# Kernel optimization log

Hardware: AMD Instinct MI355X
Metric: run time of the kernel (lower is better)

Reference implementation:

```python
import jax, jax.numpy as jnp
import numpy as np

B, L, D, H, DH = 2, 2048, 768, 12, 3072
HD = D // H          # head dim = 64
EPS = 1e-6
SCALE = float(np.sqrt(HD))


def setup_inputs() -> dict:
    key = jax.random.key(0)
    ks = jax.random.split(key, 24)
    w = lambda k, shape: jax.random.normal(k, shape, jnp.float32) * 0.02
    # RoPE angles: [L, HD//2]
    inv_freq = 1.0 / (10000.0 ** (jnp.arange(HD // 2, dtype=jnp.float32) / (HD // 2)))
    ang = jnp.arange(L, dtype=jnp.float32)[:, None] * inv_freq[None, :]
    return {
        "x": jax.random.normal(ks[0], (B, L, D), jnp.float32),
        "c": jax.random.normal(ks[1], (B, D), jnp.float32),
        "freqs_cos": jnp.cos(ang),
        "freqs_sin": jnp.sin(ang),
        "W_q": w(ks[2], (D, D)), "W_k": w(ks[3], (D, D)),
        "W_v": w(ks[4], (D, D)), "W_o": w(ks[5], (D, D)),
        "cond_w1": w(ks[6], (D, DH)), "cond_b1": jnp.zeros((DH,), jnp.float32),
        "cond_w2": w(ks[7], (DH, D)), "cond_b2": jnp.zeros((D,), jnp.float32),
        "attn_norm_w": jnp.ones((D,), jnp.float32),
        "attn_alpha": w(ks[8], (D, D)), "attn_beta": w(ks[9], (D, D)),
        "attn_gamma": w(ks[10], (D, D)),
        "ffn_gate": w(ks[11], (D, DH)), "ffn_hidden": w(ks[12], (D, DH)),
        "ffn_out": w(ks[13], (DH, D)),
        "ffn_norm_w": jnp.ones((D,), jnp.float32),
        "ffn_beta": w(ks[14], (D, D)), "ffn_gamma": w(ks[15], (D, D)),
    }


def _rms_norm(x, w):
    return w * x * jax.lax.rsqrt(jnp.mean(x * x, axis=-1, keepdims=True) + EPS)


def _rope(x, cos, sin):
    # x: [b, n, l, hd]; complex pairs are consecutive (even, odd) lanes
    x0, x1 = x[..., 0::2], x[..., 1::2]
    c, s = cos[None, None], sin[None, None]          # [1,1,l,hd//2]
    r0 = x0 * c - x1 * s
    r1 = x0 * s + x1 * c
    return jnp.stack([r0, r1], axis=-1).reshape(x.shape)


def _attention(h, cos, sin, W_q, W_k, W_v, W_o):
    b, l, d = h.shape
    split = lambda y: y.reshape(b, l, H, HD).transpose(0, 2, 1, 3)  # b n l hd
    q = _rope(split(h @ W_q), cos, sin)
    k = _rope(split(h @ W_k), cos, sin)
    v = split(h @ W_v)
    scores = jnp.einsum("bnld,bnmd->bnlm", q, k) / SCALE
    attn = jax.nn.softmax(scores, axis=-1)
    o = jnp.einsum("bnlm,bnmd->bnld", attn, v)
    return o.transpose(0, 2, 1, 3).reshape(b, l, d) @ W_o


def reference(x, c, freqs_cos, freqs_sin, W_q, W_k, W_v, W_o,
              cond_w1, cond_b1, cond_w2, cond_b2,
              attn_norm_w, attn_alpha, attn_beta, attn_gamma,
              ffn_gate, ffn_hidden, ffn_out, ffn_norm_w, ffn_beta, ffn_gamma):
    # conditioning embedding
    c2 = jax.nn.silu(c @ cond_w1 + cond_b1) @ cond_w2 + cond_b2   # [b, d]
    mod = lambda W: (c2 @ W)[:, None]                              # [b, 1, d]
    # attention sub-block with AdaLN modulation + alpha gating
    h = _rms_norm(x, attn_norm_w) * mod(attn_gamma) + mod(attn_beta)
    x = x + _attention(h, freqs_cos, freqs_sin, W_q, W_k, W_v, W_o) * mod(attn_alpha)
    # SwiGLU FFN sub-block (original gates the residual by ffn_gamma, not alpha)
    h = _rms_norm(x, ffn_norm_w) * mod(ffn_gamma) + mod(ffn_beta)
    ff = (jax.nn.silu(h @ ffn_gate) * (h @ ffn_hidden)) @ ffn_out
    return x + ff * mod(ffn_gamma)
```

## Files before the change

kernel.cpp:

```cpp
#include <hip/hip_runtime.h>

typedef unsigned short u16;
typedef __attribute__((ext_vector_type(8))) short short8;
typedef __attribute__((ext_vector_type(4))) float f32x4;

#define L_SEQ 2048
#define NHEAD 12

__device__ __forceinline__ u16 f2bf(float f) {
    union { float f; unsigned u; } x; x.f = f;
    unsigned r = x.u + 0x7fffu + ((x.u >> 16) & 1u);
    return (u16)(r >> 16);
}
__device__ __forceinline__ float bf2f(u16 u) {
    union { unsigned u; float f; } x; x.u = ((unsigned)u) << 16;
    return x.f;
}
__device__ __forceinline__ float silu_f(float x) { return x / (1.f + __expf(-x)); }

__device__ __forceinline__ void gload16(const u16* g, u16* l) {
    __builtin_amdgcn_global_load_lds(
        (const __attribute__((address_space(1))) void*)g,
        (__attribute__((address_space(3))) void*)l, 16, 0, 0);
}

__global__ __launch_bounds__(256) void transpose_convert4(
    const float* __restrict__ S0, const float* __restrict__ S1,
    const float* __restrict__ S2, const float* __restrict__ S3,
    u16* __restrict__ D0, u16* __restrict__ D1, u16* __restrict__ D2, u16* __restrict__ D3,
    int K, int N)
{
    const float* W = (blockIdx.z == 0) ? S0 : (blockIdx.z == 1) ? S1 : (blockIdx.z == 2) ? S2 : S3;
    u16* Wt = (blockIdx.z == 0) ? D0 : (blockIdx.z == 1) ? D1 : (blockIdx.z == 2) ? D2 : D3;
    __shared__ float t[32][33];
    int tx = threadIdx.x & 31, ty = threadIdx.x >> 5;
    int n0 = blockIdx.x * 32, k0 = blockIdx.y * 32;
#pragma unroll
    for (int i = 0; i < 4; i++)
        t[ty + 8 * i][tx] = W[(size_t)(k0 + ty + 8 * i) * N + n0 + tx];
    __syncthreads();
#pragma unroll
    for (int i = 0; i < 4; i++)
        Wt[(size_t)(n0 + ty + 8 * i) * K + k0 + tx] = f2bf(t[tx][ty + 8 * i]);
}

__global__ __launch_bounds__(256) void cond_mlp1(
    const float* __restrict__ c, const float* __restrict__ w1, float* __restrict__ part)
{
    int j = blockIdx.x * 256 + threadIdx.x;
    int d0 = blockIdx.y * 96;
    float a0 = 0.f, a1 = 0.f;
    for (int d = d0; d < d0 + 96; ++d) {
        float w = w1[(size_t)d * 3072 + j];
        a0 += c[d] * w;
        a1 += c[768 + d] * w;
    }
    part[(size_t)(blockIdx.y * 2 + 0) * 3072 + j] = a0;
    part[(size_t)(blockIdx.y * 2 + 1) * 3072 + j] = a1;
}

__global__ __launch_bounds__(256) void cond_mlp2(
    const float* __restrict__ part, const float* __restrict__ b1,
    const float* __restrict__ w2, float* __restrict__ c2part)
{
    __shared__ float hid[2][384];
    const int tid = threadIdx.x;
    const int d0 = blockIdx.y * 384;
    for (int i = tid; i < 768; i += 256) {
        int b = i / 384, dd = i - b * 384;
        float s = b1[d0 + dd];
#pragma unroll
        for (int p = 0; p < 8; p++) s += part[(size_t)(p * 2 + b) * 3072 + d0 + dd];
        hid[b][dd] = silu_f(s);
    }
    __syncthreads();
    int jj = tid & 63, kc = tid >> 6;
    int j = blockIdx.x * 64 + jj;
    float a0 = 0.f, a1 = 0.f;
    for (int dd = kc * 96; dd < kc * 96 + 96; ++dd) {
        float w = w2[(size_t)(d0 + dd) * 768 + j];
        a0 += hid[0][dd] * w;
        a1 += hid[1][dd] * w;
    }
    __shared__ float r0[256], r1[256];
    r0[tid] = a0; r1[tid] = a1;
    __syncthreads();
    if (kc == 0) {
        a0 = r0[jj] + r0[64 + jj] + r0[128 + jj] + r0[192 + jj];
        a1 = r1[jj] + r1[64 + jj] + r1[128 + jj] + r1[192 + jj];
        c2part[(size_t)(blockIdx.y * 2 + 0) * 768 + j] = a0;
        c2part[(size_t)(blockIdx.y * 2 + 1) * 768 + j] = a1;
    }
}

__global__ __launch_bounds__(256) void mod_gemm(
    const float* __restrict__ c2part, const float* __restrict__ b2,
    const float* __restrict__ W0, const float* __restrict__ W1,
    const float* __restrict__ W2, const float* __restrict__ W3,
    const float* __restrict__ W4, float* __restrict__ out)
{
    __shared__ float c2s[2][768];
    const int tid = threadIdx.x;
    for (int i = tid; i < 1536; i += 256) {
        int b = i / 768, d = i - b * 768;
        float s = b2[d];
#pragma unroll
        for (int p = 0; p < 8; p++) s += c2part[(size_t)(p * 2 + b) * 768 + d];
        c2s[b][d] = s;
    }
    __syncthreads();
    int w = blockIdx.y;
    const float* W = (w == 0) ? W0 : (w == 1) ? W1 : (w == 2) ? W2 : (w == 3) ? W3 : W4;
    int jj = tid & 63, kc = tid >> 6;
    int j = blockIdx.x * 64 + jj;
    float a0 = 0.f, a1 = 0.f;
    for (int d = kc * 192; d < kc * 192 + 192; ++d) {
        float ww = W[(size_t)d * 768 + j];
        a0 += c2s[0][d] * ww;
        a1 += c2s[1][d] * ww;
    }
    __shared__ float r0[256], r1[256];
    r0[tid] = a0; r1[tid] = a1;
    __syncthreads();
    if (kc == 0) {
        a0 = r0[jj] + r0[64 + jj] + r0[128 + jj] + r0[192 + jj];
        a1 = r1[jj] + r1[64 + jj] + r1[128 + jj] + r1[192 + jj];
        out[(size_t)(w * 2 + 0) * 768 + j] = a0;
        out[(size_t)(w * 2 + 1) * 768 + j] = a1;
    }
}

__global__ __launch_bounds__(256) void rmsnorm_mod(
    const float* __restrict__ xin, const float* __restrict__ nw,
    const float* __restrict__ gamma, const float* __restrict__ beta,
    u16* __restrict__ hout)
{
    int row = blockIdx.x;
    int b = row >> 11;
    const float* xr = xin + (size_t)row * 768;
    int t = threadIdx.x;
    float v0 = xr[t], v1 = xr[t + 256], v2 = xr[t + 512];
    float ss = v0 * v0 + v1 * v1 + v2 * v2;
#pragma unroll
    for (int m = 1; m < 64; m <<= 1) ss += __shfl_xor(ss, m);
    __shared__ float red[4];
    if ((t & 63) == 0) red[t >> 6] = ss;
    __syncthreads();
    float tot = red[0] + red[1] + red[2] + red[3];
    float rr = rsqrtf(tot * (1.f / 768.f) + 1e-6f);
    u16* ho = hout + (size_t)row * 768;
    const float* g = gamma + (size_t)b * 768;
    const float* be = beta + (size_t)b * 768;
#pragma unroll
    for (int i = 0; i < 3; i++) {
        int col = t + i * 256;
        float v = (i == 0) ? v0 : (i == 1) ? v1 : v2;
        ho[col] = f2bf(v * rr * nw[col] * g[col] + be[col]);
    }
}

template<int BM, int WM, int MODE>
__global__ __launch_bounds__(256) void gemm_bf16(
    const u16* __restrict__ A,
    const u16* __restrict__ B0, const u16* __restrict__ B1, const u16* __restrict__ B2,
    float* __restrict__ Cf, u16* __restrict__ Cb,
    const float* __restrict__ X, const float* __restrict__ coef,
    int M, int N, int K)
{
    constexpr int MR = WM / 16, NR = 4;
    __shared__ __align__(16) u16 As[2][BM * 32];
    __shared__ __align__(16) u16 Bs[2][128 * 32];
    const u16* Bt = (blockIdx.z == 0) ? B0 : ((blockIdx.z == 1) ? B1 : B2);
    const size_t zoff = (size_t)blockIdx.z * (size_t)M * (size_t)N;
    const int tid = threadIdx.x;
    const int lane = tid & 63, wid = tid >> 6;
    const int lo = lane & 15, hi = lane >> 4;
    const int bm = blockIdx.x * BM, bn = blockIdx.y * 128;
    const int wrow = (wid >> 1) * WM, wcol = (wid & 1) * 64;

    f32x4 acc[MR][NR];
#pragma unroll
    for (int a = 0; a < MR; a++)
#pragma unroll
        for (int b = 0; b < NR; b++)
            acc[a][b] = (f32x4){0.f, 0.f, 0.f, 0.f};

    auto stage = [&](int buf, int k0) {
#pragma unroll
        for (int p = 0; p < BM / 64; p++) {
            int ch = tid + p * 256;
            gload16(A + (size_t)(bm + (ch >> 2)) * K + k0 + (ch & 3) * 8, &As[buf][ch * 8]);
        }
#pragma unroll
        for (int p = 0; p < 2; p++) {
            int ch = tid + p * 256;
            gload16(Bt + (size_t)(bn + (ch >> 2)) * K + k0 + (ch & 3) * 8, &Bs[buf][ch * 8]);
        }
    };

    stage(0, 0);
    int cur = 0;
    const int NT = K >> 5;
    for (int t = 0; t < NT; t++) {
        __syncthreads();
        if (t + 1 < NT) stage(cur ^ 1, (t + 1) * 32);
        short8 af[MR], bfr[NR];
#pragma unroll
        for (int mi = 0; mi < MR; mi++)
            af[mi] = *(const short8*)(&As[cur][(wrow + mi * 16 + lo) * 32 + hi * 8]);
#pragma unroll
        for (int nj = 0; nj < NR; nj++)
            bfr[nj] = *(const short8*)(&Bs[cur][(wcol + nj * 16 + lo) * 32 + hi * 8]);
        __builtin_amdgcn_s_setprio(1);
#pragma unroll
        for (int mi = 0; mi < MR; mi++)
#pragma unroll
            for (int nj = 0; nj < NR; nj++)
                acc[mi][nj] = __builtin_amdgcn_mfma_f32_16x16x32_bf16(af[mi], bfr[nj], acc[mi][nj], 0, 0, 0);
        __builtin_amdgcn_s_setprio(0);
        cur ^= 1;
    }
#pragma unroll
    for (int mi = 0; mi < MR; mi++)
#pragma unroll
        for (int nj = 0; nj < NR; nj++)
#pragma unroll
            for (int i = 0; i < 4; i++) {
                int row = bm + wrow + mi * 16 + hi * 4 + i;
                int col = bn + wcol + nj * 16 + lo;
                size_t idx = (size_t)row * N + col;
                float v = acc[mi][nj][i];
                if (MODE == 1) {
                    Cb[zoff + idx] = f2bf(v);
                } else {
                    int b = row >> 11;
                    Cf[idx] = X[idx] + v * coef[(size_t)b * N + col];
                }
            }
}

__global__ __launch_bounds__(256) void gemm_ffn1(
    const u16* __restrict__ A, const u16* __restrict__ Gt, const u16* __restrict__ Ht,
    u16* __restrict__ ff, int M, int N, int K)
{
    __shared__ __align__(16) u16 As[2][128 * 32];
    __shared__ __align__(16) u16 Gs[2][64 * 32];
    __shared__ __align__(16) u16 Hs[2][64 * 32];
    const int tid = threadIdx.x;
    const int lane = tid & 63, wid = tid >> 6;
    const int lo = lane & 15, hi = lane >> 4;
    const int bm = blockIdx.x * 128, bn = blockIdx.y * 64;
    const int wrow = (wid >> 1) * 64, wcol = (wid & 1) * 32;

    f32x4 ag[4][2], ah[4][2];
#pragma unroll
    for (int a = 0; a < 4; a++)
#pragma unroll
        for (int b = 0; b < 2; b++) {
            ag[a][b] = (f32x4){0.f, 0.f, 0.f, 0.f};
            ah[a][b] = (f32x4){0.f, 0.f, 0.f, 0.f};
        }

    auto stage = [&](int buf, int k0) {
#pragma unroll
        for (int p = 0; p < 2; p++) {
            int ch = tid + p * 256;
            gload16(A + (size_t)(bm + (ch >> 2)) * K + k0 + (ch & 3) * 8, &As[buf][ch * 8]);
        }
        {
            int ch = tid;
            gload16(Gt + (size_t)(bn + (ch >> 2)) * K + k0 + (ch & 3) * 8, &Gs[buf][ch * 8]);
            gload16(Ht + (size_t)(bn + (ch >> 2)) * K + k0 + (ch & 3) * 8, &Hs[buf][ch * 8]);
        }
    };

    stage(0, 0);
    int cur = 0;
    const int NT = K >> 5;
    for (int t = 0; t < NT; t++) {
        __syncthreads();
        if (t + 1 < NT) stage(cur ^ 1, (t + 1) * 32);
        short8 af[4], gf[2], hf[2];
#pragma unroll
        for (int mi = 0; mi < 4; mi++)
            af[mi] = *(const short8*)(&As[cur][(wrow + mi * 16 + lo) * 32 + hi * 8]);
#pragma unroll
        for (int nj = 0; nj < 2; nj++) {
            gf[nj] = *(const short8*)(&Gs[cur][(wcol + nj * 16 + lo) * 32 + hi * 8]);
            hf[nj] = *(const short8*)(&Hs[cur][(wcol + nj * 16 + lo) * 32 + hi * 8]);
        }
        __builtin_amdgcn_s_setprio(1);
#pragma unroll
        for (int mi = 0; mi < 4; mi++)
#pragma unroll
            for (int nj = 0; nj < 2; nj++) {
                ag[mi][nj] = __builtin_amdgcn_mfma_f32_16x16x32_bf16(af[mi], gf[nj], ag[mi][nj], 0, 0, 0);
                ah[mi][nj] = __builtin_amdgcn_mfma_f32_16x16x32_bf16(af[mi], hf[nj], ah[mi][nj], 0, 0, 0);
            }
        __builtin_amdgcn_s_setprio(0);
        cur ^= 1;
    }
#pragma unroll
    for (int mi = 0; mi < 4; mi++)
#pragma unroll
        for (int nj = 0; nj < 2; nj++)
#pragma unroll
            for (int i = 0; i < 4; i++) {
                int row = bm + wrow + mi * 16 + hi * 4 + i;
                int col = bn + wcol + nj * 16 + lo;
                ff[(size_t)row * N + col] = f2bf(silu_f(ag[mi][nj][i]) * ah[mi][nj][i]);
            }
}

__global__ __launch_bounds__(256) void rope_reshape(
    const u16* __restrict__ qr, const u16* __restrict__ kr, const u16* __restrict__ vr,
    const float* __restrict__ fc, const float* __restrict__ fs,
    u16* __restrict__ qo, u16* __restrict__ ko, u16* __restrict__ vt)
{
    const float QSCALE = 0.125f * 1.44269504f;
    __shared__ u16 Vl[64 * 64];
    const int tid = threadIdx.x;
    const int bh = blockIdx.y, lt = blockIdx.x;
    const int b = bh / NHEAD, h = bh % NHEAD;
    const int l0 = lt * 64;
    const int lrow = tid >> 2, ch = tid & 3;

    const size_t srow = ((size_t)(b * L_SEQ + l0 + lrow)) * 768 + h * 64 + ch * 16;
    const size_t drow = ((size_t)(bh * L_SEQ + l0 + lrow)) * 64 + ch * 16;

    float cs[8], sn[8];
#pragma unroll
    for (int i = 0; i < 8; i++) {
        cs[i] = fc[(l0 + lrow) * 32 + ch * 8 + i];
        sn[i] = fs[(l0 + lrow) * 32 + ch * 8 + i];
    }
    union { int4 v4[2]; u16 s[16]; } iv, ov;
    iv.v4[0] = *(const int4*)(qr + srow); iv.v4[1] = *(const int4*)(qr + srow + 8);
#pragma unroll
    for (int i = 0; i < 8; i++) {
        float x0 = bf2f(iv.s[2 * i]), x1 = bf2f(iv.s[2 * i + 1]);
        ov.s[2 * i]     = f2bf((x0 * cs[i] - x1 * sn[i]) * QSCALE);
        ov.s[2 * i + 1] = f2bf((x0 * sn[i] + x1 * cs[i]) * QSCALE);
    }
    *(int4*)(qo + drow) = ov.v4[0]; *(int4*)(qo + drow + 8) = ov.v4[1];
    iv.v4[0] = *(const int4*)(kr + srow); iv.v4[1] = *(const int4*)(kr + srow + 8);
#pragma unroll
    for (int i = 0; i < 8; i++) {
        float x0 = bf2f(iv.s[2 * i]), x1 = bf2f(iv.s[2 * i + 1]);
        ov.s[2 * i]     = f2bf(x0 * cs[i] - x1 * sn[i]);
        ov.s[2 * i + 1] = f2bf(x0 * sn[i] + x1 * cs[i]);
    }
    *(int4*)(ko + drow) = ov.v4[0]; *(int4*)(ko + drow + 8) = ov.v4[1];
    iv.v4[0] = *(const int4*)(vr + srow); iv.v4[1] = *(const int4*)(vr + srow + 8);
#pragma unroll
    for (int e = 0; e < 16; e++) {
        int d = ch * 16 + e;
        Vl[d * 64 + (lrow ^ (((d >> 3) & 7) << 3))] = iv.s[e];
    }
    __syncthreads();
    const int d = tid >> 2;
    const int key = ((d >> 3) & 7) << 3;
    int4 o0 = *(const int4*)(&Vl[d * 64 + ((ch * 16) ^ key)]);
    int4 o1 = *(const int4*)(&Vl[d * 64 + ((ch * 16 + 8) ^ key)]);
    u16* vd = vt + ((size_t)bh * 64 + d) * L_SEQ + l0 + ch * 16;
    *(int4*)(vd) = o0; *(int4*)(vd + 8) = o1;
}

__global__ __launch_bounds__(256) void attn_fwd(
    const u16* __restrict__ q, const u16* __restrict__ k, const u16* __restrict__ vt,
    u16* __restrict__ outp)
{
    __shared__ __align__(16) u16 Kb[2][64 * 64];
    __shared__ __align__(16) u16 Vb[2][64 * 64];
    __shared__ __align__(16) u16 Ps[4][16 * 64];
    const int tid = threadIdx.x;
    const int lane = tid & 63, wid = tid >> 6;
    const int lo = lane & 15, hi = lane >> 4;
    const int qt = blockIdx.x, bh = blockIdx.y;
    const int b = bh / NHEAD, h = bh % NHEAD;
    const int q0 = qt * 64 + wid * 16;
    const u16* qb = q + ((size_t)bh * L_SEQ + q0) * 64;
    const u16* kbase = k + (size_t)bh * L_SEQ * 64;
    const u16* vbase = vt + (size_t)bh * 64 * L_SEQ;

    short8 qa0 = *(const short8*)(qb + lo * 64 + hi * 8);
    short8 qa1 = *(const short8*)(qb + lo * 64 + 32 + hi * 8);

    f32x4 oacc[4];
#pragma unroll
    for (int dt = 0; dt < 4; dt++) oacc[dt] = (f32x4){0.f, 0.f, 0.f, 0.f};
    float m_ = -1e30f, ls = 0.f;

    auto stage = [&](int buf, int kv0) {
#pragma unroll
        for (int p = 0; p < 2; p++) {
            int chk = tid + p * 256;
            int r = chk >> 3;
            int sl = (chk & 7) ^ (r & 7);
            gload16(kbase + (size_t)(kv0 + r) * 64 + sl * 8, &Kb[buf][chk * 8]);
        }
#pragma unroll
        for (int p = 0; p < 2; p++) {
            int chk = tid + p * 256;
            int r = chk >> 3;
            int sl = (chk & 7) ^ (r & 7);
            gload16(vbase + (size_t)r * L_SEQ + kv0 + sl * 8, &Vb[buf][chk * 8]);
        }
    };

    stage(0, 0);
    int cur = 0;
    u16* pw = &Ps[wid][0];
    const int pkey = (lo & 7) << 3;
    for (int t = 0; t < L_SEQ / 64; t++) {
        __syncthreads();
        if (t + 1 < L_SEQ / 64) stage(cur ^ 1, (t + 1) * 64);
        f32x4 s[4];
#pragma unroll
        for (int nt = 0; nt < 4; nt++) {
            int kr = nt * 16 + lo;
            const u16* kp = &Kb[cur][kr * 64];
            short8 kf0 = *(const short8*)(kp + ((hi * 8) ^ pkey));
            short8 kf1 = *(const short8*)(kp + ((32 + hi * 8) ^ pkey));
            __builtin_amdgcn_s_setprio(1);
            f32x4 z = (f32x4){0.f, 0.f, 0.f, 0.f};
            z = __builtin_amdgcn_mfma_f32_16x16x32_bf16(kf0, qa0, z, 0, 0, 0);
            s[nt] = __builtin_amdgcn_mfma_f32_16x16x32_bf16(kf1, qa1, s[nt] = z, 0, 0, 0);
            __builtin_amdgcn_s_setprio(0);
        }
        float t0 = fmaxf(fmaxf(s[0][0], s[0][1]), fmaxf(s[0][2], s[0][3]));
        float t1 = fmaxf(fmaxf(s[1][0], s[1][1]), fmaxf(s[1][2], s[1][3]));
        float t2 = fmaxf(fmaxf(s[2][0], s[2][1]), fmaxf(s[2][2], s[2][3]));
        float t3 = fmaxf(fmaxf(s[3][0], s[3][1]), fmaxf(s[3][2], s[3][3]));
        float pmax = fmaxf(fmaxf(t0, t1), fmaxf(t2, t3));
        pmax = fmaxf(pmax, __shfl_xor(pmax, 16));
        pmax = fmaxf(pmax, __shfl_xor(pmax, 32));
        if (!__all(pmax - m_ <= 8.f)) {
            float mn = fmaxf(m_, pmax);
            float al = exp2f(m_ - mn);
            m_ = mn;
            ls *= al;
#pragma unroll
            for (int dt = 0; dt < 4; dt++) oacc[dt] *= al;
        }
        float rs = 0.f;
#pragma unroll
        for (int nt = 0; nt < 4; nt++)
#pragma unroll
            for (int r = 0; r < 4; r++) {
                float p = exp2f(s[nt][r] - m_);
                s[nt][r] = p;
                rs += p;
            }
        rs += __shfl_xor(rs, 16);
        rs += __shfl_xor(rs, 32);
        ls += rs;
#pragma unroll
        for (int nt = 0; nt < 4; nt++) {
            unsigned w0, w1;
            asm("v_cvt_pk_bf16_f32 %0, %1, %2" : "=v"(w0) : "v"(s[nt][0]), "v"(s[nt][1]));
            asm("v_cvt_pk_bf16_f32 %0, %1, %2" : "=v"(w1) : "v"(s[nt][2]), "v"(s[nt][3]));
            uint2 pk2; pk2.x = w0; pk2.y = w1;
            *(uint2*)(pw + lo * 64 + ((nt * 16 + hi * 4) ^ pkey)) = pk2;
        }
        short8 pa0 = *(const short8*)(pw + lo * 64 + ((hi * 8) ^ pkey));
        short8 pa1 = *(const short8*)(pw + lo * 64 + ((32 + hi * 8) ^ pkey));
#pragma unroll
        for (int dt = 0; dt < 4; dt++) {
            int vr_ = dt * 16 + lo;
            const u16* vp = &Vb[cur][vr_ * 64];
            short8 vf0 = *(const short8*)(vp + ((hi * 8) ^ pkey));
            short8 vf1 = *(const short8*)(vp + ((32 + hi * 8) ^ pkey));
            __builtin_amdgcn_s_setprio(1);
            oacc[dt] = __builtin_amdgcn_mfma_f32_16x16x32_bf16(vf0, pa0, oacc[dt], 0, 0, 0);
            oacc[dt] = __builtin_amdgcn_mfma_f32_16x16x32_bf16(vf1, pa1, oacc[dt], 0, 0, 0);
            __builtin_amdgcn_s_setprio(0);
        }
        cur ^= 1;
    }
    float inv = 1.f / ls;
    int qrow = q0 + lo;
    u16* orow = outp + ((size_t)(b * L_SEQ + qrow)) * 768 + h * 64;
#pragma unroll
    for (int dt = 0; dt < 4; dt++)
#pragma unroll
        for (int r = 0; r < 4; r++)
            orow[dt * 16 + hi * 4 + r] = f2bf(oacc[dt][r] * inv);
}

extern "C" void kernel_launch(void* const* d_in, const int* in_sizes, int n_in,
                              void* d_out, int out_size, void* d_ws, size_t ws_size,
                              hipStream_t stream)
{
    const float* x      = (const float*)d_in[0];
    const float* c      = (const float*)d_in[1];
    const float* fcos   = (const float*)d_in[2];
    const float* fsin   = (const float*)d_in[3];
    const float* Wq     = (const float*)d_in[4];
    const float* Wk     = (const float*)d_in[5];
    const float* Wv     = (const float*)d_in[6];
    const float* Wo     = (const float*)d_in[7];
    const float* cw1    = (const float*)d_in[8];
    const float* cb1    = (const float*)d_in[9];
    const float* cw2    = (const float*)d_in[10];
    const float* cb2    = (const float*)d_in[11];
    const float* anw    = (const float*)d_in[12];
    const float* Walpha = (const float*)d_in[13];
    const float* Wbeta  = (const float*)d_in[14];
    const float* Wgamma = (const float*)d_in[15];
    const float* Wgate  = (const float*)d_in[16];
    const float* Whid   = (const float*)d_in[17];
    const float* Wout   = (const float*)d_in[18];
    const float* fnw    = (const float*)d_in[19];
    const float* Wbetaf = (const float*)d_in[20];
    const float* Wgammaf= (const float*)d_in[21];

    const int M = 4096;
    char* ws = (char*)d_ws;
    size_t off = 0;
    auto alloc = [&](size_t bytes) -> char* {
        char* p = ws + off;
        off += (bytes + 255) & ~(size_t)255;
        return p;
    };
    u16* wq_t   = (u16*)alloc((size_t)768 * 768 * 2);
    u16* wk_t   = (u16*)alloc((size_t)768 * 768 * 2);
    u16* wv_t   = (u16*)alloc((size_t)768 * 768 * 2);
    u16* wo_t   = (u16*)alloc((size_t)768 * 768 * 2);
    u16* gate_t = (u16*)alloc((size_t)3072 * 768 * 2);
    u16* hid_t  = (u16*)alloc((size_t)3072 * 768 * 2);
    u16* out_t  = (u16*)alloc((size_t)768 * 3072 * 2);
    float* part1 = (float*)alloc((size_t)8 * 2 * 3072 * 4);
    float* part2 = (float*)alloc((size_t)8 * 2 * 768 * 4);
    float* mods = (float*)alloc(5 * 2 * 768 * 4);
    u16* hbuf   = (u16*)alloc((size_t)M * 768 * 2);
    u16* qkvraw = (u16*)alloc((size_t)3 * M * 768 * 2);
    u16* qrope  = (u16*)alloc((size_t)M * 768 * 2);
    u16* krope  = (u16*)alloc((size_t)M * 768 * 2);
    u16* vtb    = (u16*)alloc((size_t)M * 768 * 2);
    u16* attnh  = (u16*)alloc((size_t)M * 768 * 2);
    float* ybuf = (float*)alloc((size_t)M * 768 * 4);
    u16* ffbuf  = (u16*)alloc((size_t)M * 3072 * 2);

    transpose_convert4<<<dim3(24, 24, 4), 256, 0, stream>>>(
        Wq, Wk, Wv, Wo, wq_t, wk_t, wv_t, wo_t, 768, 768);
    transpose_convert4<<<dim3(96, 24, 2), 256, 0, stream>>>(
        Wgate, Whid, Wgate, Whid, gate_t, hid_t, gate_t, hid_t, 768, 3072);
    transpose_convert4<<<dim3(24, 96, 1), 256, 0, stream>>>(
        Wout, Wout, Wout, Wout, out_t, out_t, out_t, out_t, 3072, 768);

    cond_mlp1<<<dim3(12, 8), 256, 0, stream>>>(c, cw1, part1);
    cond_mlp2<<<dim3(12, 8), 256, 0, stream>>>(part1, cb1, cw2, part2);
    mod_gemm<<<dim3(12, 5), 256, 0, stream>>>(
        part2, cb2, Wgamma, Wbeta, Walpha, Wgammaf, Wbetaf, mods);

    rmsnorm_mod<<<M, 256, 0, stream>>>(x, anw, mods + 0 * 1536, mods + 1 * 1536, hbuf);

    gemm_bf16<128, 64, 1><<<dim3(32, 6, 3), 256, 0, stream>>>(
        hbuf, wq_t, wk_t, wv_t, nullptr, qkvraw, nullptr, nullptr, M, 768, 768);

    rope_reshape<<<dim3(32, 24), 256, 0, stream>>>(
        qkvraw, qkvraw + (size_t)M * 768, qkvraw + (size_t)2 * M * 768,
        fcos, fsin, qrope, krope, vtb);

    attn_fwd<<<dim3(32, 24), 256, 0, stream>>>(qrope, krope, vtb, attnh);

    gemm_bf16<64, 32, 2><<<dim3(64, 6, 1), 256, 0, stream>>>(
        attnh, wo_t, wo_t, wo_t, ybuf, nullptr, x, mods + 2 * 1536, M, 768, 768);

    rmsnorm_mod<<<M, 256, 0, stream>>>(ybuf, fnw, mods + 3 * 1536, mods + 4 * 1536, hbuf);

    gemm_ffn1<<<dim3(32, 48), 256, 0, stream>>>(
        hbuf, gate_t, hid_t, ffbuf, M, 3072, 768);

    gemm_bf16<64, 32, 2><<<dim3(64, 6, 1), 256, 0, stream>>>(
        ffbuf, out_t, out_t, out_t, (float*)d_out, nullptr, ybuf, mods + 3 * 1536, M, 768, 3072);
}
```

Measured before the change: 271.7 us.

## Fuse QKV into one wide GEMM and double attention KV tile to 128

```diff
diff --git a/kernel.cpp b/kernel.cpp
--- a/kernel.cpp
+++ b/kernel.cpp
@@ -6,6 +6,7 @@
 
 #define L_SEQ 2048
 #define NHEAD 12
+#define KVB 128
 
 __device__ __forceinline__ u16 f2bf(float f) {
     union { float f; unsigned u; } x; x.f = f;
@@ -161,8 +162,7 @@
 
 template<int BM, int WM, int MODE>
 __global__ __launch_bounds__(256) void gemm_bf16(
-    const u16* __restrict__ A,
-    const u16* __restrict__ B0, const u16* __restrict__ B1, const u16* __restrict__ B2,
+    const u16* __restrict__ A, const u16* __restrict__ Bt,
     float* __restrict__ Cf, u16* __restrict__ Cb,
     const float* __restrict__ X, const float* __restrict__ coef,
     int M, int N, int K)
@@ -170,8 +170,6 @@
     constexpr int MR = WM / 16, NR = 4;
     __shared__ __align__(16) u16 As[2][BM * 32];
     __shared__ __align__(16) u16 Bs[2][128 * 32];
-    const u16* Bt = (blockIdx.z == 0) ? B0 : ((blockIdx.z == 1) ? B1 : B2);
-    const size_t zoff = (size_t)blockIdx.z * (size_t)M * (size_t)N;
     const int tid = threadIdx.x;
     const int lane = tid & 63, wid = tid >> 6;
     const int lo = lane & 15, hi = lane >> 4;
@@ -231,7 +229,7 @@
                 size_t idx = (size_t)row * N + col;
                 float v = acc[mi][nj][i];
                 if (MODE == 1) {
-                    Cb[zoff + idx] = f2bf(v);
+                    Cb[idx] = f2bf(v);
                 } else {
                     int b = row >> 11;
                     Cf[idx] = X[idx] + v * coef[(size_t)b * N + col];
@@ -325,7 +323,7 @@
     const int l0 = lt * 64;
     const int lrow = tid >> 2, ch = tid & 3;
 
-    const size_t srow = ((size_t)(b * L_SEQ + l0 + lrow)) * 768 + h * 64 + ch * 16;
+    const size_t srow = ((size_t)(b * L_SEQ + l0 + lrow)) * 2304 + h * 64 + ch * 16;
     const size_t drow = ((size_t)(bh * L_SEQ + l0 + lrow)) * 64 + ch * 16;
 
     float cs[8], sn[8];
@@ -370,9 +368,9 @@
     const u16* __restrict__ q, const u16* __restrict__ k, const u16* __restrict__ vt,
     u16* __restrict__ outp)
 {
-    __shared__ __align__(16) u16 Kb[2][64 * 64];
-    __shared__ __align__(16) u16 Vb[2][64 * 64];
-    __shared__ __align__(16) u16 Ps[4][16 * 64];
+    __shared__ __align__(16) u16 Kb[2][KVB * 64];
+    __shared__ __align__(16) u16 Vb[2][64 * KVB];
+    __shared__ __align__(16) u16 Ps[4][16 * KVB];
     const int tid = threadIdx.x;
     const int lane = tid & 63, wid = tid >> 6;
     const int lo = lane & 15, hi = lane >> 4;
@@ -393,18 +391,18 @@
 
     auto stage = [&](int buf, int kv0) {
 #pragma unroll
-        for (int p = 0; p < 2; p++) {
+        for (int p = 0; p < 4; p++) {
             int chk = tid + p * 256;
             int r = chk >> 3;
             int sl = (chk & 7) ^ (r & 7);
             gload16(kbase + (size_t)(kv0 + r) * 64 + sl * 8, &Kb[buf][chk * 8]);
         }
 #pragma unroll
-        for (int p = 0; p < 2; p++) {
+        for (int p = 0; p < 4; p++) {
             int chk = tid + p * 256;
-            int r = chk >> 3;
-            int sl = (chk & 7) ^ (r & 7);
-            gload16(vbase + (size_t)r * L_SEQ + kv0 + sl * 8, &Vb[buf][chk * 8]);
+            int r = chk >> 4;
+            int cc = (chk & 15) ^ (r & 7);
+            gload16(vbase + (size_t)r * L_SEQ + kv0 + cc * 8, &Vb[buf][chk * 8]);
         }
     };
 
@@ -412,27 +410,29 @@
     int cur = 0;
     u16* pw = &Ps[wid][0];
     const int pkey = (lo & 7) << 3;
-    for (int t = 0; t < L_SEQ / 64; t++) {
+    for (int t = 0; t < L_SEQ / KVB; t++) {
         __syncthreads();
-        if (t + 1 < L_SEQ / 64) stage(cur ^ 1, (t + 1) * 64);
-        f32x4 s[4];
-#pragma unroll
-        for (int nt = 0; nt < 4; nt++) {
+        if (t + 1 < L_SEQ / KVB) stage(cur ^ 1, (t + 1) * KVB);
+        f32x4 s[8];
+#pragma unroll
+        for (int nt = 0; nt < 8; nt++) {
             int kr = nt * 16 + lo;
             const u16* kp = &Kb[cur][kr * 64];
-            short8 kf0 = *(const short8*)(kp + ((hi * 8) ^ pkey));
-            short8 kf1 = *(const short8*)(kp + ((32 + hi * 8) ^ pkey));
+            int key = (kr & 7) << 3;
+            short8 kf0 = *(const short8*)(kp + ((hi * 8) ^ key));
+            short8 kf1 = *(const short8*)(kp + ((32 + hi * 8) ^ key));
             __builtin_amdgcn_s_setprio(1);
             f32x4 z = (f32x4){0.f, 0.f, 0.f, 0.f};
             z = __builtin_amdgcn_mfma_f32_16x16x32_bf16(kf0, qa0, z, 0, 0, 0);
             s[nt] = __builtin_amdgcn_mfma_f32_16x16x32_bf16(kf1, qa1, s[nt] = z, 0, 0, 0);
             __builtin_amdgcn_s_setprio(0);
         }
-        float t0 = fmaxf(fmaxf(s[0][0], s[0][1]), fmaxf(s[0][2], s[0][3]));
-        float t1 = fmaxf(fmaxf(s[1][0], s[1][1]), fmaxf(s[1][2], s[1][3]));
-        float t2 = fmaxf(fmaxf(s[2][0], s[2][1]), fmaxf(s[2][2], s[2][3]));
-        float t3 = fmaxf(fmaxf(s[3][0], s[3][1]), fmaxf(s[3][2], s[3][3]));
-        float pmax = fmaxf(fmaxf(t0, t1), fmaxf(t2, t3));
+        float pmax = -1e30f;
+#pragma unroll
+        for (int nt = 0; nt < 8; nt++) {
+            float tn = fmaxf(fmaxf(s[nt][0], s[nt][1]), fmaxf(s[nt][2], s[nt][3]));
+            pmax = fmaxf(pmax, tn);
+        }
         pmax = fmaxf(pmax, __shfl_xor(pmax, 16));
         pmax = fmaxf(pmax, __shfl_xor(pmax, 32));
         if (!__all(pmax - m_ <= 8.f)) {
@@ -445,7 +445,7 @@
         }
         float rs = 0.f;
 #pragma unroll
-        for (int nt = 0; nt < 4; nt++)
+        for (int nt = 0; nt < 8; nt++)
 #pragma unroll
             for (int r = 0; r < 4; r++) {
                 float p = exp2f(s[nt][r] - m_);
@@ -456,24 +456,28 @@
         rs += __shfl_xor(rs, 32);
         ls += rs;
 #pragma unroll
-        for (int nt = 0; nt < 4; nt++) {
+        for (int nt = 0; nt < 8; nt++) {
             unsigned w0, w1;
             asm("v_cvt_pk_bf16_f32 %0, %1, %2" : "=v"(w0) : "v"(s[nt][0]), "v"(s[nt][1]));
             asm("v_cvt_pk_bf16_f32 %0, %1, %2" : "=v"(w1) : "v"(s[nt][2]), "v"(s[nt][3]));
             uint2 pk2; pk2.x = w0; pk2.y = w1;
-            *(uint2*)(pw + lo * 64 + ((nt * 16 + hi * 4) ^ pkey)) = pk2;
-        }
-        short8 pa0 = *(const short8*)(pw + lo * 64 + ((hi * 8) ^ pkey));
-        short8 pa1 = *(const short8*)(pw + lo * 64 + ((32 + hi * 8) ^ pkey));
+            *(uint2*)(pw + lo * KVB + ((nt * 16 + hi * 4) ^ pkey)) = pk2;
+        }
+        short8 pa[4];
+#pragma unroll
+        for (int kk = 0; kk < 4; kk++)
+            pa[kk] = *(const short8*)(pw + lo * KVB + ((kk * 32 + hi * 8) ^ pkey));
 #pragma unroll
         for (int dt = 0; dt < 4; dt++) {
             int vr_ = dt * 16 + lo;
-            const u16* vp = &Vb[cur][vr_ * 64];
-            short8 vf0 = *(const short8*)(vp + ((hi * 8) ^ pkey));
-            short8 vf1 = *(const short8*)(vp + ((32 + hi * 8) ^ pkey));
+            const u16* vp = &Vb[cur][vr_ * KVB];
+            int vkey = (vr_ & 7) << 3;
             __builtin_amdgcn_s_setprio(1);
-            oacc[dt] = __builtin_amdgcn_mfma_f32_16x16x32_bf16(vf0, pa0, oacc[dt], 0, 0, 0);
-            oacc[dt] = __builtin_amdgcn_mfma_f32_16x16x32_bf16(vf1, pa1, oacc[dt], 0, 0, 0);
+#pragma unroll
+            for (int kk = 0; kk < 4; kk++) {
+                short8 vf = *(const short8*)(vp + ((kk * 32 + hi * 8) ^ vkey));
+                oacc[dt] = __builtin_amdgcn_mfma_f32_16x16x32_bf16(vf, pa[kk], oacc[dt], 0, 0, 0);
+            }
             __builtin_amdgcn_s_setprio(0);
         }
         cur ^= 1;
@@ -534,7 +538,7 @@
     float* part2 = (float*)alloc((size_t)8 * 2 * 768 * 4);
     float* mods = (float*)alloc(5 * 2 * 768 * 4);
     u16* hbuf   = (u16*)alloc((size_t)M * 768 * 2);
-    u16* qkvraw = (u16*)alloc((size_t)3 * M * 768 * 2);
+    u16* qkvraw = (u16*)alloc((size_t)M * 2304 * 2);
     u16* qrope  = (u16*)alloc((size_t)M * 768 * 2);
     u16* krope  = (u16*)alloc((size_t)M * 768 * 2);
     u16* vtb    = (u16*)alloc((size_t)M * 768 * 2);
@@ -556,17 +560,17 @@
 
     rmsnorm_mod<<<M, 256, 0, stream>>>(x, anw, mods + 0 * 1536, mods + 1 * 1536, hbuf);
 
-    gemm_bf16<128, 64, 1><<<dim3(32, 6, 3), 256, 0, stream>>>(
-        hbuf, wq_t, wk_t, wv_t, nullptr, qkvraw, nullptr, nullptr, M, 768, 768);
+    gemm_bf16<128, 64, 1><<<dim3(32, 18, 1), 256, 0, stream>>>(
+        hbuf, wq_t, nullptr, qkvraw, nullptr, nullptr, M, 2304, 768);
 
     rope_reshape<<<dim3(32, 24), 256, 0, stream>>>(
-        qkvraw, qkvraw + (size_t)M * 768, qkvraw + (size_t)2 * M * 768,
+        qkvraw, qkvraw + 768, qkvraw + 1536,
         fcos, fsin, qrope, krope, vtb);
 
     attn_fwd<<<dim3(32, 24), 256, 0, stream>>>(qrope, krope, vtb, attnh);
 
     gemm_bf16<64, 32, 2><<<dim3(64, 6, 1), 256, 0, stream>>>(
-        attnh, wo_t, wo_t, wo_t, ybuf, nullptr, x, mods + 2 * 1536, M, 768, 768);
+        attnh, wo_t, ybuf, nullptr, x, mods + 2 * 1536, M, 768, 768);
 
     rmsnorm_mod<<<M, 256, 0, stream>>>(ybuf, fnw, mods + 3 * 1536, mods + 4 * 1536, hbuf);
 
@@ -574,5 +578,5 @@
         hbuf, gate_t, hid_t, ffbuf, M, 3072, 768);
 
     gemm_bf16<64, 32, 2><<<dim3(64, 6, 1), 256, 0, stream>>>(
-        ffbuf, out_t, out_t, out_t, (float*)d_out, nullptr, ybuf, mods + 3 * 1536, M, 768, 3072);
-}
+        ffbuf, out_t, (float*)d_out, nullptr, ybuf, mods + 3 * 1536, M, 768, 3072);
+}
```

Measured after the change: 298.6 us. 9.9% more time.

## Fuse QKV into one wide GEMM, swizzle attention blocks by XCD, pack bf16 stores

Applied to the files above, without the earlier changes.

```diff
diff --git a/kernel.cpp b/kernel.cpp
--- a/kernel.cpp
+++ b/kernel.cpp
@@ -161,8 +161,7 @@
 
 template<int BM, int WM, int MODE>
 __global__ __launch_bounds__(256) void gemm_bf16(
-    const u16* __restrict__ A,
-    const u16* __restrict__ B0, const u16* __restrict__ B1, const u16* __restrict__ B2,
+    const u16* __restrict__ A, const u16* __restrict__ Bt,
     float* __restrict__ Cf, u16* __restrict__ Cb,
     const float* __restrict__ X, const float* __restrict__ coef,
     int M, int N, int K)
@@ -170,8 +169,6 @@
     constexpr int MR = WM / 16, NR = 4;
     __shared__ __align__(16) u16 As[2][BM * 32];
     __shared__ __align__(16) u16 Bs[2][128 * 32];
-    const u16* Bt = (blockIdx.z == 0) ? B0 : ((blockIdx.z == 1) ? B1 : B2);
-    const size_t zoff = (size_t)blockIdx.z * (size_t)M * (size_t)N;
     const int tid = threadIdx.x;
     const int lane = tid & 63, wid = tid >> 6;
     const int lo = lane & 15, hi = lane >> 4;
@@ -231,7 +228,7 @@
                 size_t idx = (size_t)row * N + col;
                 float v = acc[mi][nj][i];
                 if (MODE == 1) {
-                    Cb[zoff + idx] = f2bf(v);
+                    Cb[idx] = f2bf(v);
                 } else {
                     int b = row >> 11;
                     Cf[idx] = X[idx] + v * coef[(size_t)b * N + col];
@@ -325,7 +322,7 @@
     const int l0 = lt * 64;
     const int lrow = tid >> 2, ch = tid & 3;
 
-    const size_t srow = ((size_t)(b * L_SEQ + l0 + lrow)) * 768 + h * 64 + ch * 16;
+    const size_t srow = ((size_t)(b * L_SEQ + l0 + lrow)) * 2304 + h * 64 + ch * 16;
     const size_t drow = ((size_t)(bh * L_SEQ + l0 + lrow)) * 64 + ch * 16;
 
     float cs[8], sn[8];
@@ -376,7 +373,10 @@
     const int tid = threadIdx.x;
     const int lane = tid & 63, wid = tid >> 6;
     const int lo = lane & 15, hi = lane >> 4;
-    const int qt = blockIdx.x, bh = blockIdx.y;
+    const int lid = blockIdx.x;
+    const int xcd = lid & 7, li = lid >> 3;
+    const int bh = xcd * 3 + (li >> 5);
+    const int qt = li & 31;
     const int b = bh / NHEAD, h = bh % NHEAD;
     const int q0 = qt * 64 + wid * 16;
     const u16* qb = q + ((size_t)bh * L_SEQ + q0) * 64;
@@ -482,10 +482,15 @@
     int qrow = q0 + lo;
     u16* orow = outp + ((size_t)(b * L_SEQ + qrow)) * 768 + h * 64;
 #pragma unroll
-    for (int dt = 0; dt < 4; dt++)
-#pragma unroll
-        for (int r = 0; r < 4; r++)
-            orow[dt * 16 + hi * 4 + r] = f2bf(oacc[dt][r] * inv);
+    for (int dt = 0; dt < 4; dt++) {
+        unsigned w0, w1;
+        float o0 = oacc[dt][0] * inv, o1 = oacc[dt][1] * inv;
+        float o2 = oacc[dt][2] * inv, o3 = oacc[dt][3] * inv;
+        asm("v_cvt_pk_bf16_f32 %0, %1, %2" : "=v"(w0) : "v"(o0), "v"(o1));
+        asm("v_cvt_pk_bf16_f32 %0, %1, %2" : "=v"(w1) : "v"(o2), "v"(o3));
+        uint2 pk2; pk2.x = w0; pk2.y = w1;
+        *(uint2*)(orow + dt * 16 + hi * 4) = pk2;
+    }
 }
 
 extern "C" void kernel_launch(void* const* d_in, const int* in_sizes, int n_in,
@@ -534,7 +539,7 @@
     float* part2 = (float*)alloc((size_t)8 * 2 * 768 * 4);
     float* mods = (float*)alloc(5 * 2 * 768 * 4);
     u16* hbuf   = (u16*)alloc((size_t)M * 768 * 2);
-    u16* qkvraw = (u16*)alloc((size_t)3 * M * 768 * 2);
+    u16* qkvraw = (u16*)alloc((size_t)M * 2304 * 2);
     u16* qrope  = (u16*)alloc((size_t)M * 768 * 2);
     u16* krope  = (u16*)alloc((size_t)M * 768 * 2);
     u16* vtb    = (u16*)alloc((size_t)M * 768 * 2);
@@ -556,17 +561,17 @@
 
     rmsnorm_mod<<<M, 256, 0, stream>>>(x, anw, mods + 0 * 1536, mods + 1 * 1536, hbuf);
 
-    gemm_bf16<128, 64, 1><<<dim3(32, 6, 3), 256, 0, stream>>>(
-        hbuf, wq_t, wk_t, wv_t, nullptr, qkvraw, nullptr, nullptr, M, 768, 768);
+    gemm_bf16<128, 64, 1><<<dim3(32, 18, 1), 256, 0, stream>>>(
+        hbuf, wq_t, nullptr, qkvraw, nullptr, nullptr, M, 2304, 768);
 
     rope_reshape<<<dim3(32, 24), 256, 0, stream>>>(
-        qkvraw, qkvraw + (size_t)M * 768, qkvraw + (size_t)2 * M * 768,
+        qkvraw, qkvraw + 768, qkvraw + 1536,
         fcos, fsin, qrope, krope, vtb);
 
-    attn_fwd<<<dim3(32, 24), 256, 0, stream>>>(qrope, krope, vtb, attnh);
+    attn_fwd<<<dim3(768), 256, 0, stream>>>(qrope, krope, vtb, attnh);
 
     gemm_bf16<64, 32, 2><<<dim3(64, 6, 1), 256, 0, stream>>>(
-        attnh, wo_t, wo_t, wo_t, ybuf, nullptr, x, mods + 2 * 1536, M, 768, 768);
+        attnh, wo_t, ybuf, nullptr, x, mods + 2 * 1536, M, 768, 768);
 
     rmsnorm_mod<<<M, 256, 0, stream>>>(ybuf, fnw, mods + 3 * 1536, mods + 4 * 1536, hbuf);
 
@@ -574,5 +579,5 @@
         hbuf, gate_t, hid_t, ffbuf, M, 3072, 768);
 
     gemm_bf16<64, 32, 2><<<dim3(64, 6, 1), 256, 0, stream>>>(
-        ffbuf, out_t, out_t, out_t, (float*)d_out, nullptr, ybuf, mods + 3 * 1536, M, 768, 3072);
-}
+        ffbuf, out_t, (float*)d_out, nullptr, ybuf, mods + 3 * 1536, M, 768, 3072);
+}
```

Measured after the change: 270.9 us. No clear change (-0.3%).
